# Kernel tuning notes

Hardware: AMD Instinct MI355X
Metric: run time of the kernel (lower is better)

Reference implementation:

```python
import jax, jax.numpy as jnp
import numpy as np

INPUT_SIZE = 64
STATE_SIZE = 1984
OUTPUT_SIZE = 64
WIDTH = INPUT_SIZE + STATE_SIZE  # 2048
ID_PROP = 0.9
SEQ_LEN = 128
BATCH = 128


def setup_inputs() -> dict:
    key = jax.random.key(0)
    k1, k2, k3 = jax.random.split(key, 3)
    # xavier-uniform bound for square [WIDTH, WIDTH] linears
    bound = float(np.sqrt(6.0 / (WIDTH + WIDTH)))
    W1 = jax.random.uniform(k1, (WIDTH, WIDTH), jnp.float32, -bound, bound)
    W2 = jax.random.uniform(k2, (WIDTH, WIDTH), jnp.float32, -bound, bound)
    b1 = jnp.zeros((WIDTH,), jnp.float32)
    b2 = jnp.zeros((WIDTH,), jnp.float32)
    inp = jax.random.normal(k3, (SEQ_LEN, BATCH, INPUT_SIZE), jnp.float32)
    return {"input": inp, "W1": W1, "b1": b1, "W2": W2, "b2": b2}


def reference(input, W1, b1, W2, b2):
    T, B, _ = input.shape
    # initial output_stream is zeros of width WIDTH, broadcast over batch
    state0 = jnp.zeros((B, WIDTH), input.dtype)

    def step(state, x_t):
        # Shift: concat(input, state) then keep first WIDTH elems
        s = jnp.concatenate([x_t, state[:, :STATE_SIZE]], axis=-1)  # [B, WIDTH]
        # Res: r*p + (1-p) * fc2(|fc1(s)|)
        h = jnp.abs(s @ W1.T + b1)
        s = s * ID_PROP + (1.0 - ID_PROP) * (h @ W2.T + b2)
        return s, None

    state, _ = jax.lax.scan(step, state0, input)
    return state[..., -OUTPUT_SIZE:]
```

## Files before the change

### kernel.cpp

```cpp
#include <hip/hip_runtime.h>
#include <stdint.h>


#define NSTEPS 128
#define NB 128
#define WID 2048
#define SS 1984

typedef __attribute__((ext_vector_type(8))) short short8;
typedef __attribute__((ext_vector_type(4))) short short4v;
typedef __attribute__((ext_vector_type(4))) float f32x4;
typedef unsigned long long u64;

static __device__ __forceinline__ short f2bf(float f) {
  union { float f; unsigned u; } v; v.f = f;
  unsigned r = (v.u + 0x7fffu + ((v.u >> 16) & 1u)) >> 16;
  return (short)r;
}

static __device__ __forceinline__ short8 pack8(f32x4 lo, f32x4 hi) {
  short8 r;
  r[0] = f2bf(lo[0]); r[1] = f2bf(lo[1]); r[2] = f2bf(lo[2]); r[3] = f2bf(lo[3]);
  r[4] = f2bf(hi[0]); r[5] = f2bf(hi[1]); r[6] = f2bf(hi[2]); r[7] = f2bf(hi[3]);
  return r;
}

static __device__ __forceinline__ void ast64(void* p, u64 v) {
  __hip_atomic_store((u64*)p, v, __ATOMIC_RELAXED, __HIP_MEMORY_SCOPE_AGENT);
}
static __device__ __forceinline__ unsigned ald32(const unsigned* p) {
  return __hip_atomic_load(p, __ATOMIC_RELAXED, __HIP_MEMORY_SCOPE_AGENT);
}

#define LLCLD(d, a) \
  asm volatile("global_load_dwordx4 %0, %1, off sc1" : "=&v"(d) : "v"(a))
#define VMW(n) do { \
    asm volatile("s_waitcnt vmcnt(" #n ")" ::: "memory"); \
    __builtin_amdgcn_sched_barrier(0); \
  } while (0)

#define CLD(d, a, bit, msk) do {                                              \
    if ((msk) & (1u << (bit))) {                                              \
      asm volatile("global_load_dwordx4 %0, %1, off sc0" : "=&v"(d) : "v"(a));\
    } else {                                                                  \
      asm volatile("global_load_dwordx4 %0, %1, off sc1" : "=&v"(d) : "v"(a));\
    }                                                                         \
  } while (0)

#define P1ISSUE(b, X) do {                                                    \
    if (kb == 0 && (b) == 0) {   \
      const float* q0_ = inp + ((size_t)t * NB + m0) * 64 + q8;               \
      const float* q1_ = inp + ((size_t)t * NB + m1) * 64 + q8;               \
      X[0] = pack8(*(const f32x4*)q0_, *(const f32x4*)(q0_ + 4));             \
      X[1] = pack8(*(const f32x4*)q1_, *(const f32x4*)(q1_ + 4));             \
      X[2] = pack8(*(const f32x4*)(q0_ + 32), *(const f32x4*)(q0_ + 36));     \
      X[3] = pack8(*(const f32x4*)(q1_ + 32), *(const f32x4*)(q1_ + 36));     \
      const short* s_ = SbOld + (size_t)slabL * 1024;                         \
      CLD(X[4], (s_ + rowoff0),        2, m1s);                               \
      CLD(X[5], (s_ + rowoff1),        2, m1s);                               \
      CLD(X[6], (s_ + 4096 + rowoff0), 3, m1s);                               \
      CLD(X[7], (s_ + 4096 + rowoff1), 3, m1s);                               \
    } else {                                                                  \
      const short* s_ = SbOld + (size_t)(kb / 8 + 16 * (b) - 8 + slabL) * 1024; \
      CLD(X[0], (s_ + rowoff0),         4*(b)+0, m1s);                        \
      CLD(X[1], (s_ + rowoff1),         4*(b)+0, m1s);                        \
      CLD(X[2], (s_ + 4096 + rowoff0),  4*(b)+1, m1s);                        \
      CLD(X[3], (s_ + 4096 + rowoff1),  4*(b)+1, m1s);                        \
      CLD(X[4], (s_ + 8192 + rowoff0),  4*(b)+2, m1s);                        \
      CLD(X[5], (s_ + 8192 + rowoff1),  4*(b)+2, m1s);                        \
      CLD(X[6], (s_ + 12288 + rowoff0), 4*(b)+3, m1s);                        \
      CLD(X[7], (s_ + 12288 + rowoff1), 4*(b)+3, m1s);                        \
    }                                                                         \
  } while (0)

#define P1MFMA(b, X) do {                                                     \
    a00 = __builtin_amdgcn_mfma_f32_16x16x32_bf16(X[0], B1[4*(b)+0][0], a00, 0,0,0); \
    a01 = __builtin_amdgcn_mfma_f32_16x16x32_bf16(X[0], B1[4*(b)+0][1], a01, 0,0,0); \
    a10 = __builtin_amdgcn_mfma_f32_16x16x32_bf16(X[1], B1[4*(b)+0][0], a10, 0,0,0); \
    a11 = __builtin_amdgcn_mfma_f32_16x16x32_bf16(X[1], B1[4*(b)+0][1], a11, 0,0,0); \
    a00 = __builtin_amdgcn_mfma_f32_16x16x32_bf16(X[2], B1[4*(b)+1][0], a00, 0,0,0); \
    a01 = __builtin_amdgcn_mfma_f32_16x16x32_bf16(X[2], B1[4*(b)+1][1], a01, 0,0,0); \
    a10 = __builtin_amdgcn_mfma_f32_16x16x32_bf16(X[3], B1[4*(b)+1][0], a10, 0,0,0); \
    a11 = __builtin_amdgcn_mfma_f32_16x16x32_bf16(X[3], B1[4*(b)+1][1], a11, 0,0,0); \
    a00 = __builtin_amdgcn_mfma_f32_16x16x32_bf16(X[4], B1[4*(b)+2][0], a00, 0,0,0); \
    a01 = __builtin_amdgcn_mfma_f32_16x16x32_bf16(X[4], B1[4*(b)+2][1], a01, 0,0,0); \
    a10 = __builtin_amdgcn_mfma_f32_16x16x32_bf16(X[5], B1[4*(b)+2][0], a10, 0,0,0); \
    a11 = __builtin_amdgcn_mfma_f32_16x16x32_bf16(X[5], B1[4*(b)+2][1], a11, 0,0,0); \
    a00 = __builtin_amdgcn_mfma_f32_16x16x32_bf16(X[6], B1[4*(b)+3][0], a00, 0,0,0); \
    a01 = __builtin_amdgcn_mfma_f32_16x16x32_bf16(X[6], B1[4*(b)+3][1], a01, 0,0,0); \
    a10 = __builtin_amdgcn_mfma_f32_16x16x32_bf16(X[7], B1[4*(b)+3][0], a10, 0,0,0); \
    a11 = __builtin_amdgcn_mfma_f32_16x16x32_bf16(X[7], B1[4*(b)+3][1], a11, 0,0,0); \
  } while (0)

#define P2ISSUE(b, X) do {                                                    \
    const short* h_ = hb + (size_t)(kb / 8 + 16 * (b) + slabL) * 1024;        \
    CLD(X[0], (h_ + rowoff0),         4*(b)+0, m2s);                          \
    CLD(X[1], (h_ + rowoff1),         4*(b)+0, m2s);                          \
    CLD(X[2], (h_ + 4096 + rowoff0),  4*(b)+1, m2s);                          \
    CLD(X[3], (h_ + 4096 + rowoff1),  4*(b)+1, m2s);                          \
    CLD(X[4], (h_ + 8192 + rowoff0),  4*(b)+2, m2s);                          \
    CLD(X[5], (h_ + 8192 + rowoff1),  4*(b)+2, m2s);                          \
    CLD(X[6], (h_ + 12288 + rowoff0), 4*(b)+3, m2s);                          \
    CLD(X[7], (h_ + 12288 + rowoff1), 4*(b)+3, m2s);                          \
  } while (0)

#define P2MFMA(b, X) do {                                                     \
    c00 = __builtin_amdgcn_mfma_f32_16x16x32_bf16(X[0], B2[4*(b)+0][0], c00, 0,0,0); \
    c01 = __builtin_amdgcn_mfma_f32_16x16x32_bf16(X[0], B2[4*(b)+0][1], c01, 0,0,0); \
    c10 = __builtin_amdgcn_mfma_f32_16x16x32_bf16(X[1], B2[4*(b)+0][0], c10, 0,0,0); \
    c11 = __builtin_amdgcn_mfma_f32_16x16x32_bf16(X[1], B2[4*(b)+0][1], c11, 0,0,0); \
    c00 = __builtin_amdgcn_mfma_f32_16x16x32_bf16(X[2], B2[4*(b)+1][0], c00, 0,0,0); \
    c01 = __builtin_amdgcn_mfma_f32_16x16x32_bf16(X[2], B2[4*(b)+1][1], c01, 0,0,0); \
    c10 = __builtin_amdgcn_mfma_f32_16x16x32_bf16(X[3], B2[4*(b)+1][0], c10, 0,0,0); \
    c11 = __builtin_amdgcn_mfma_f32_16x16x32_bf16(X[3], B2[4*(b)+1][1], c11, 0,0,0); \
    c00 = __builtin_amdgcn_mfma_f32_16x16x32_bf16(X[4], B2[4*(b)+2][0], c00, 0,0,0); \
    c01 = __builtin_amdgcn_mfma_f32_16x16x32_bf16(X[4], B2[4*(b)+2][1], c01, 0,0,0); \
    c10 = __builtin_amdgcn_mfma_f32_16x16x32_bf16(X[5], B2[4*(b)+2][0], c10, 0,0,0); \
    c11 = __builtin_amdgcn_mfma_f32_16x16x32_bf16(X[5], B2[4*(b)+2][1], c11, 0,0,0); \
    c00 = __builtin_amdgcn_mfma_f32_16x16x32_bf16(X[6], B2[4*(b)+3][0], c00, 0,0,0); \
    c01 = __builtin_amdgcn_mfma_f32_16x16x32_bf16(X[6], B2[4*(b)+3][1], c01, 0,0,0); \
    c10 = __builtin_amdgcn_mfma_f32_16x16x32_bf16(X[7], B2[4*(b)+3][0], c10, 0,0,0); \
    c11 = __builtin_amdgcn_mfma_f32_16x16x32_bf16(X[7], B2[4*(b)+3][1], c11, 0,0,0); \
  } while (0)

__global__ __launch_bounds__(256, 1)
void resrnn_kernel(const float* __restrict__ inp, const float* __restrict__ W1,
                   const float* __restrict__ b1f, const float* __restrict__ W2,
                   const float* __restrict__ b2f, float* __restrict__ out,
                   unsigned char* __restrict__ ws)
{
  const int tid   = threadIdx.x;
  const int bid   = blockIdx.x;
  const int group = bid & 3;
  const int chunk = bid >> 2;
  const int mbase = group * 32;
  const int n0    = chunk * 32;
  const int wave  = tid >> 6;
  const int lane  = tid & 63;
  const int l15   = lane & 15;
  const int q8    = (lane >> 4) * 8;
  const int kb    = wave * 512;
  const int slabL = lane >> 4;

  unsigned* sgen = (unsigned*)(ws + group * 8192);
  unsigned* hgen = (unsigned*)(ws + group * 8192 + 4096);
  unsigned* xtab = (unsigned*)(ws + 32768);
  unsigned* verd = (unsigned*)(ws + 33792);
  float* Sf0  = (float*)(ws + 36864);
  float* Sf1  = (float*)(ws + 36864 + 1015808);
  short* Sb0  = (short*)(ws + 36864 + 2031616);
  short* Sb1  = (short*)(ws + 36864 + 2539520);
  short* hb   = (short*)(ws + 36864 + 3047424);

  __shared__ float red[4][16][65];
  __shared__ unsigned hcnt[10];

  unsigned xraw;
  asm("s_getreg_b32 %0, hwreg(HW_REG_XCC_ID)" : "=s"(xraw));
  const unsigned myx = xraw + 1u;
  if (tid == 0)
    __hip_atomic_store(xtab + bid, myx, __ATOMIC_RELAXED, __HIP_MEMORY_SCOPE_AGENT);
  if (bid == 0) {
    unsigned v;
    for (;;) { v = ald32(xtab + tid); if (v) break; __builtin_amdgcn_s_sleep(2); }
    if (tid < 10) hcnt[tid] = 0;
    __syncthreads();
    atomicAdd(&hcnt[v <= 8 ? v : 0], 1u);
    __syncthreads();
    if (tid == 0) {
      bool ok = (hcnt[0] == 0);
      for (int q = 1; q <= 8; ++q) if (hcnt[q] != 32) ok = false;
      __hip_atomic_store(verd, ok ? 1u : 2u, __ATOMIC_RELAXED, __HIP_MEMORY_SCOPE_AGENT);
    }
  }

  short8 B1[16][2], B2[16][2];
#pragma unroll
  for (int ks = 0; ks < 16; ++ks) {
#pragma unroll
    for (int nt = 0; nt < 2; ++nt) {
      const float* p1 = W1 + (size_t)(n0 + nt * 16 + l15) * WID + (kb + ks * 32 + q8);
      B1[ks][nt] = pack8(*(const f32x4*)p1, *(const f32x4*)(p1 + 4));
      const float* p2 = W2 + (size_t)(n0 + nt * 16 + l15) * WID + (kb + ks * 32 + q8);
      B2[ks][nt] = pack8(*(const f32x4*)p2, *(const f32x4*)(p2 + 4));
    }
  }

  unsigned vd;
  for (;;) { vd = ald32(verd); if (vd) break; __builtin_amdgcn_s_sleep(2); }
  unsigned m1v = 0, m2v = 0;
  if (vd == 1) {
    for (int j = 0; j < 16; ++j) {
      const int p2c = 16 * wave + j;
      if (ald32(xtab + ((p2c << 2) | group)) == myx) m2v |= 1u << j;
      const int p1c = p2c - 2;
      if (p1c >= 0 && ald32(xtab + ((p1c << 2) | group)) == myx) m1v |= 1u << j;
    }
  }
  const unsigned m1s = __builtin_amdgcn_readfirstlane(m1v);
  const unsigned m2s = __builtin_amdgcn_readfirstlane(m2v);
  const bool locPrev = (__builtin_amdgcn_readfirstlane(vd) == 1u);

  const int m0 = mbase + l15;
  const int m1 = mbase + 16 + l15;
  const int rowoff0 = (mbase + l15) * 8;
  const int rowoff1 = rowoff0 + 128;

  const int ml   = (tid & 63) >> 1;
  const int nl   = ((tid >> 6) << 3) + ((tid & 1) << 2);
  const int mrow = mbase + ml;
  const int c0   = n0 + nl;
  const size_t toff = (size_t)(n0 / 8 + wave) * 1024 + (size_t)mrow * 8
                    + (size_t)((tid & 1) << 2);

  const f32x4 b1r = *(const f32x4*)(b1f + c0);
  const f32x4 b2r = *(const f32x4*)(b2f + c0);

  const int p1pc = 16 * wave + l15 - 2;
  const bool p1needA = (lane < 16) && (p1pc >= 0);
  const bool p1needB = (lane == 16) && (chunk >= 2);
  const unsigned* p1fp =
      p1needA ? (sgen + p1pc * 16)
              : (sgen + (chunk >= 2 ? chunk - 2 : 0) * 16);
  const unsigned* p2fp = hgen + (16 * wave + l15) * 16;

  short8 xa[8], xb[8], xc[8], xd[8];

#pragma unroll 1
  for (int t = 0; t < NSTEPS; ++t) {
    const float* SfOld = (t & 1) ? Sf1 : Sf0;
    float*       SfNew = (t & 1) ? Sf0 : Sf1;
    const short* SbOld = (t & 1) ? Sb1 : Sb0;
    short*       SbNew = (t & 1) ? Sb0 : Sb1;

    f32x4 a00{}, a01{}, a10{}, a11{};
    f32x4 prevv;
    if (t == 0) {
      prevv = (c0 < 64) ? *(const f32x4*)(inp + (size_t)mrow * 64 + c0)
                        : f32x4{0.f, 0.f, 0.f, 0.f};
      if (kb == 0) {
        const float* q0_ = inp + (size_t)m0 * 64 + q8;
        const float* q1_ = inp + (size_t)m1 * 64 + q8;
        short8 x0 = pack8(*(const f32x4*)q0_, *(const f32x4*)(q0_ + 4));
        short8 x1 = pack8(*(const f32x4*)q1_, *(const f32x4*)(q1_ + 4));
        short8 x2 = pack8(*(const f32x4*)(q0_ + 32), *(const f32x4*)(q0_ + 36));
        short8 x3 = pack8(*(const f32x4*)(q1_ + 32), *(const f32x4*)(q1_ + 36));
        a00 = __builtin_amdgcn_mfma_f32_16x16x32_bf16(x0, B1[0][0], a00, 0, 0, 0);
        a01 = __builtin_amdgcn_mfma_f32_16x16x32_bf16(x0, B1[0][1], a01, 0, 0, 0);
        a10 = __builtin_amdgcn_mfma_f32_16x16x32_bf16(x1, B1[0][0], a10, 0, 0, 0);
        a11 = __builtin_amdgcn_mfma_f32_16x16x32_bf16(x1, B1[0][1], a11, 0, 0, 0);
        a00 = __builtin_amdgcn_mfma_f32_16x16x32_bf16(x2, B1[1][0], a00, 0, 0, 0);
        a01 = __builtin_amdgcn_mfma_f32_16x16x32_bf16(x2, B1[1][1], a01, 0, 0, 0);
        a10 = __builtin_amdgcn_mfma_f32_16x16x32_bf16(x3, B1[1][0], a10, 0, 0, 0);
        a11 = __builtin_amdgcn_mfma_f32_16x16x32_bf16(x3, B1[1][1], a11, 0, 0, 0);
      }
    } else {
      {
        const unsigned tgt = (unsigned)t;
        bool pend = p1needA || p1needB;
        for (;;) {
          if (pend && ald32(p1fp) >= tgt) pend = false;
          if (__ballot(pend) == 0ull) break;
        }
      }
      if (chunk < 2) {
        prevv = *(const f32x4*)(inp + ((size_t)t * NB + mrow) * 64 + c0);
        P1ISSUE(0, xa); P1ISSUE(1, xb); P1ISSUE(2, xc); P1ISSUE(3, xd);
        VMW(24); P1MFMA(0, xa);
        VMW(16); P1MFMA(1, xb);
        VMW(8);  P1MFMA(2, xc);
        VMW(0);  P1MFMA(3, xd);
      } else {
        P1ISSUE(0, xa); P1ISSUE(1, xb); P1ISSUE(2, xc); P1ISSUE(3, xd);
        if (locPrev) {
          asm volatile("global_load_dwordx4 %0, %1, off sc0"
                       : "=&v"(prevv) : "v"(SfOld + toff - 8192));
        } else {
          LLCLD(prevv, (SfOld + toff - 8192));
        }
        VMW(25); P1MFMA(0, xa);
        VMW(17); P1MFMA(1, xb);
        VMW(9);  P1MFMA(2, xc);
        VMW(1);  P1MFMA(3, xd);
      }
    }
#pragma unroll
    for (int r = 0; r < 4; ++r) {
      red[wave][r][lane]      = a00[r];
      red[wave][4 + r][lane]  = a01[r];
      red[wave][8 + r][lane]  = a10[r];
      red[wave][12 + r][lane] = a11[r];
    }
    __syncthreads();
    {
      short4v hv;
#pragma unroll
      for (int j = 0; j < 4; ++j) {
        const int nn   = nl + j;
        const int lidx = ((ml >> 2) & 3) * 16 + (nn & 15);
        const int ridx = (ml >> 4) * 8 + (nn >> 4) * 4 + (ml & 3);
        float s = red[0][ridx][lidx] + red[1][ridx][lidx]
                + red[2][ridx][lidx] + red[3][ridx][lidx];
        s += b1r[j];
        hv[j] = f2bf(fabsf(s));
      }
      union { short4v s; u64 u; } hu; hu.s = hv;
      ast64(hb + toff, hu.u);
    }
    __syncthreads();
    if (tid == 0)
      __hip_atomic_store(hgen + chunk * 16, (unsigned)t + 1,
                         __ATOMIC_RELAXED, __HIP_MEMORY_SCOPE_AGENT);

    f32x4 c00{}, c01{}, c10{}, c11{};
    {
      {
        const unsigned tgt = (unsigned)t + 1;
        bool pend = (lane < 16);
        for (;;) {
          if (pend && ald32(p2fp) >= tgt) pend = false;
          if (__ballot(pend) == 0ull) break;
        }
      }
      P2ISSUE(0, xa); P2ISSUE(1, xb); P2ISSUE(2, xc); P2ISSUE(3, xd);
      VMW(24); P2MFMA(0, xa);
      VMW(16); P2MFMA(1, xb);
      VMW(8);  P2MFMA(2, xc);
      VMW(0);  P2MFMA(3, xd);
    }
#pragma unroll
    for (int r = 0; r < 4; ++r) {
      red[wave][r][lane]      = c00[r];
      red[wave][4 + r][lane]  = c01[r];
      red[wave][8 + r][lane]  = c10[r];
      red[wave][12 + r][lane] = c11[r];
    }
    __syncthreads();
    if (t < NSTEPS - 1) {
      if (n0 < SS) {
        f32x4 gv;
#pragma unroll
        for (int j = 0; j < 4; ++j) {
          const int nn   = nl + j;
          const int lidx = ((ml >> 2) & 3) * 16 + (nn & 15);
          const int ridx = (ml >> 4) * 8 + (nn >> 4) * 4 + (ml & 3);
          gv[j] = red[0][ridx][lidx] + red[1][ridx][lidx]
                + red[2][ridx][lidx] + red[3][ridx][lidx] + b2r[j];
        }
        f32x4 sv; short4v sb;
#pragma unroll
        for (int j = 0; j < 4; ++j) {
          float vv = 0.9f * prevv[j] + 0.1f * gv[j];
          sv[j] = vv; sb[j] = f2bf(vv);
        }
        union { f32x4 f; u64 u[2]; } sfu; sfu.f = sv;
        float* pf = SfNew + toff;
        ast64(pf, sfu.u[0]);
        ast64(pf + 2, sfu.u[1]);
        union { short4v s; u64 u; } sbu; sbu.s = sb;
        ast64(SbNew + toff, sbu.u);
      }
      __syncthreads();
      if (tid == 0 && chunk < 62)
        __hip_atomic_store(sgen + chunk * 16, (unsigned)t + 1,
                           __ATOMIC_RELAXED, __HIP_MEMORY_SCOPE_AGENT);
    } else {
      if (n0 >= SS) {
        f32x4 gv;
#pragma unroll
        for (int j = 0; j < 4; ++j) {
          const int nn   = nl + j;
          const int lidx = ((ml >> 2) & 3) * 16 + (nn & 15);
          const int ridx = (ml >> 4) * 8 + (nn >> 4) * 4 + (ml & 3);
          gv[j] = red[0][ridx][lidx] + red[1][ridx][lidx]
                + red[2][ridx][lidx] + red[3][ridx][lidx] + b2r[j];
        }
        f32x4 ov;
#pragma unroll
        for (int j = 0; j < 4; ++j) ov[j] = 0.9f * prevv[j] + 0.1f * gv[j];
        *(f32x4*)(out + (size_t)mrow * 64 + (c0 - SS)) = ov;
      }
    }
  }
}

extern "C" void kernel_launch(void* const* d_in, const int* in_sizes, int n_in,
                              void* d_out, int out_size, void* d_ws, size_t ws_size,
                              hipStream_t stream)
{
  (void)in_sizes; (void)n_in; (void)out_size; (void)ws_size;
  const float* inp = (const float*)d_in[0];
  const float* W1  = (const float*)d_in[1];
  const float* b1  = (const float*)d_in[2];
  const float* W2  = (const float*)d_in[3];
  const float* b2  = (const float*)d_in[4];
  float* out = (float*)d_out;

  hipMemsetAsync(d_ws, 0, 34048, stream);
  resrnn_kernel<<<dim3(256), dim3(256), 0, stream>>>(
      inp, W1, b1, W2, b2, out, (unsigned char*)d_ws);
}
```

Baseline: 1.088 ms.

## Split generation flags into local and remote copies with a release fence

```diff
diff --git a/kernel.cpp b/kernel.cpp
--- a/kernel.cpp
+++ b/kernel.cpp
@@ -25,8 +25,8 @@
   return r;
 }
 
-static __device__ __forceinline__ void ast64(void* p, u64 v) {
-  __hip_atomic_store((u64*)p, v, __ATOMIC_RELAXED, __HIP_MEMORY_SCOPE_AGENT);
+static __device__ __forceinline__ void aflag(unsigned* p, unsigned v) {
+  __hip_atomic_store(p, v, __ATOMIC_RELAXED, __HIP_MEMORY_SCOPE_AGENT);
 }
 static __device__ __forceinline__ unsigned ald32(const unsigned* p) {
   return __hip_atomic_load(p, __ATOMIC_RELAXED, __HIP_MEMORY_SCOPE_AGENT);
@@ -142,15 +142,17 @@
   const int kb    = wave * 512;
   const int slabL = lane >> 4;
 
-  unsigned* sgen = (unsigned*)(ws + group * 8192);
-  unsigned* hgen = (unsigned*)(ws + group * 8192 + 4096);
-  unsigned* xtab = (unsigned*)(ws + 32768);
-  unsigned* verd = (unsigned*)(ws + 33792);
-  float* Sf0  = (float*)(ws + 36864);
-  float* Sf1  = (float*)(ws + 36864 + 1015808);
-  short* Sb0  = (short*)(ws + 36864 + 2031616);
-  short* Sb1  = (short*)(ws + 36864 + 2539520);
-  short* hb   = (short*)(ws + 36864 + 3047424);
+  unsigned* sLgen = (unsigned*)(ws + group * 16384);
+  unsigned* sRgen = (unsigned*)(ws + group * 16384 + 4096);
+  unsigned* hLgen = (unsigned*)(ws + group * 16384 + 8192);
+  unsigned* hRgen = (unsigned*)(ws + group * 16384 + 12288);
+  unsigned* xtab  = (unsigned*)(ws + 65536);
+  unsigned* verd  = (unsigned*)(ws + 66560);
+  float* Sf0 = (float*)(ws + 69632);
+  float* Sf1 = (float*)(ws + 69632 + 1015808);
+  short* Sb0 = (short*)(ws + 69632 + 2031616);
+  short* Sb1 = (short*)(ws + 69632 + 2539520);
+  short* hb  = (short*)(ws + 69632 + 3047424);
 
   __shared__ float red[4][16][65];
   __shared__ unsigned hcnt[10];
@@ -158,8 +160,7 @@
   unsigned xraw;
   asm("s_getreg_b32 %0, hwreg(HW_REG_XCC_ID)" : "=s"(xraw));
   const unsigned myx = xraw + 1u;
-  if (tid == 0)
-    __hip_atomic_store(xtab + bid, myx, __ATOMIC_RELAXED, __HIP_MEMORY_SCOPE_AGENT);
+  if (tid == 0) aflag(xtab + bid, myx);
   if (bid == 0) {
     unsigned v;
     for (;;) { v = ald32(xtab + tid); if (v) break; __builtin_amdgcn_s_sleep(2); }
@@ -170,7 +171,7 @@
     if (tid == 0) {
       bool ok = (hcnt[0] == 0);
       for (int q = 1; q <= 8; ++q) if (hcnt[q] != 32) ok = false;
-      __hip_atomic_store(verd, ok ? 1u : 2u, __ATOMIC_RELAXED, __HIP_MEMORY_SCOPE_AGENT);
+      aflag(verd, ok ? 1u : 2u);
     }
   }
 
@@ -219,10 +220,12 @@
   const int p1pc = 16 * wave + l15 - 2;
   const bool p1needA = (lane < 16) && (p1pc >= 0);
   const bool p1needB = (lane == 16) && (chunk >= 2);
+  const bool p1loc = (lane < 16) ? (((m1v >> l15) & 1u) != 0u) : locPrev;
   const unsigned* p1fp =
-      p1needA ? (sgen + p1pc * 16)
-              : (sgen + (chunk >= 2 ? chunk - 2 : 0) * 16);
-  const unsigned* p2fp = hgen + (16 * wave + l15) * 16;
+      p1needA ? ((p1loc ? sLgen : sRgen) + p1pc * 16)
+              : ((p1loc ? sLgen : sRgen) + (chunk >= 2 ? chunk - 2 : 0) * 16);
+  const unsigned* p2fp =
+      (((m2v >> l15) & 1u) ? hLgen : hRgen) + (16 * wave + l15) * 16;
 
   short8 xa[8], xb[8], xc[8], xd[8];
 
@@ -305,12 +308,14 @@
         hv[j] = f2bf(fabsf(s));
       }
       union { short4v s; u64 u; } hu; hu.s = hv;
-      ast64(hb + toff, hu.u);
+      *(u64*)(hb + toff) = hu.u;
     }
     __syncthreads();
-    if (tid == 0)
-      __hip_atomic_store(hgen + chunk * 16, (unsigned)t + 1,
-                         __ATOMIC_RELAXED, __HIP_MEMORY_SCOPE_AGENT);
+    if (tid == 0) {
+      aflag(hLgen + chunk * 16, (unsigned)t + 1);
+      __builtin_amdgcn_fence(__ATOMIC_RELEASE, "agent");
+      aflag(hRgen + chunk * 16, (unsigned)t + 1);
+    }
 
     f32x4 c00{}, c01{}, c10{}, c11{};
     {
@@ -353,17 +358,16 @@
           float vv = 0.9f * prevv[j] + 0.1f * gv[j];
           sv[j] = vv; sb[j] = f2bf(vv);
         }
-        union { f32x4 f; u64 u[2]; } sfu; sfu.f = sv;
-        float* pf = SfNew + toff;
-        ast64(pf, sfu.u[0]);
-        ast64(pf + 2, sfu.u[1]);
+        *(f32x4*)(SfNew + toff) = sv;
         union { short4v s; u64 u; } sbu; sbu.s = sb;
-        ast64(SbNew + toff, sbu.u);
+        *(u64*)(SbNew + toff) = sbu.u;
       }
       __syncthreads();
-      if (tid == 0 && chunk < 62)
-        __hip_atomic_store(sgen + chunk * 16, (unsigned)t + 1,
-                           __ATOMIC_RELAXED, __HIP_MEMORY_SCOPE_AGENT);
+      if (tid == 0) {
+        if (chunk < 62) aflag(sLgen + chunk * 16, (unsigned)t + 1);
+        __builtin_amdgcn_fence(__ATOMIC_RELEASE, "agent");
+        if (chunk < 62) aflag(sRgen + chunk * 16, (unsigned)t + 1);
+      }
     } else {
       if (n0 >= SS) {
         f32x4 gv;
@@ -396,7 +400,7 @@
   const float* b2  = (const float*)d_in[4];
   float* out = (float*)d_out;
 
-  hipMemsetAsync(d_ws, 0, 34048, stream);
+  hipMemsetAsync(d_ws, 0, 69632, stream);
   resrnn_kernel<<<dim3(256), dim3(256), 0, stream>>>(
       inp, W1, b1, W2, b2, out, (unsigned char*)d_ws);
 }
```

Result: slower. 2.348 ms (+115.9%).
